# Performance work log

Measured on AMD Instinct MI355X. Metric: run time of the kernel, lower is better.

The kernel has to match this reference:

```python
import jax, jax.numpy as jnp
import numpy as np

# --- static config (matches init_kwargs) ---
N = 30000            # n_nodes
H = 8                # num_heads
OT = 16              # out_time_dim
OS = 240             # out_space_dim
IN_DIM = 16 + 1 + 240   # in_time+1 + in_space = 257
OUT_DIM = OT + 1 + OS   # 257 per head
BETA = -1.0
EPS = 1e-8
MAX_NORM = 1.0e6
SQRT_BETA = float(np.sqrt(abs(BETA)))


def setup_inputs() -> dict:
    key = jax.random.key(0)
    ks = jax.random.split(key, 7)
    def w(k, shape, fan_in):
        return (jax.random.normal(k, shape, jnp.float32) / np.sqrt(fan_in)).astype(jnp.float32)
    return {
        "query_input": jax.random.normal(ks[0], (N, IN_DIM), jnp.float32),
        "source_input": jax.random.normal(ks[1], (N, IN_DIM), jnp.float32),
        # stacked per-head PseudoLinear2 weights: [H, out, in]
        "Wq": w(ks[2], (H, OUT_DIM, IN_DIM), IN_DIM),
        "Wk": w(ks[3], (H, OUT_DIM, IN_DIM), IN_DIM),
        "Wv": w(ks[4], (H, OUT_DIM, IN_DIM), IN_DIM),
        # final head-concat projections (nn.Linear, bias=False): [out, in]
        "Ws": w(ks[5], (OT + 1, H * (OT + 1)), H * (OT + 1)),
        "Wh": w(ks[6], (OS, H * OS), H * OS),
    }


def _pseudo_linear(x, W):
    # Per-head linear; spherical block renormalized to radius sqrt(|beta|)
    # (hr output on the product manifold S^OT x H^OS). [N,D] x [H,O,D] -> [N,H,O]
    y = jnp.einsum('nd,hod->nho', x, W)
    s, sp = y[..., :OT + 1], y[..., OT + 1:]
    s = s * (SQRT_BETA / (jnp.linalg.norm(s, axis=-1, keepdims=True) + EPS))
    return jnp.concatenate([s, sp], axis=-1)


def _linear_attention(q, k, v, den_eps):
    # elu+1 feature-map linear attention; associative kv outer product per head.
    phi_q = jax.nn.elu(q) + 1.0
    phi_k = jax.nn.elu(k) + 1.0
    ktv = jnp.einsum('nhm,nhd->hmd', phi_k, v)          # [H,m,d]
    num = jnp.einsum('nhm,hmd->nhd', phi_q, ktv)        # [N,H,d]
    den = jnp.einsum('nhd,hd->nh', phi_q, phi_k.sum(0)) # [N,H]
    return num / (den[..., None] + den_eps)


def _l2norm(x):
    # torch F.normalize(p=2, dim=-1)
    return x / jnp.clip(jnp.linalg.norm(x, axis=-1, keepdims=True), 1e-12)


def reference(query_input, source_input, Wq, Wk, Wv, Ws, Wh):
    q = _pseudo_linear(query_input, Wq)   # [N,H,257]
    k = _pseudo_linear(source_input, Wk)
    v = _pseudo_linear(source_input, Wv)
    qs, qh = q[..., :OT + 1], q[..., OT + 1:]
    ks_, kh = k[..., :OT + 1], k[..., OT + 1:]
    vs, vh = v[..., :OT + 1], v[..., OT + 1:]

    # ---- spherical linear attention ----
    a = _linear_attention(qs, ks_, vs, 1e-6)            # [N,H,OT+1]
    a = a.reshape(N, H * (OT + 1)) @ Ws.T               # heads_concat
    an = jnp.linalg.norm(a, axis=-1, keepdims=True) + EPS
    mask = (an > MAX_NORM).astype(a.dtype)
    an_c = jnp.minimum(an, MAX_NORM)
    a_ = (a / an_c) * mask + a * (1.0 - mask)
    att_s = SQRT_BETA * _l2norm(a_)                     # [N,OT+1]

    # ---- hyperbolic linear attention ----
    b = _linear_attention(qh, kh, vh, 1e-8)             # [N,H,OS]
    b = b.reshape(N, H * OS) @ Wh.T
    bn = jnp.linalg.norm(b, axis=-1, keepdims=True) + EPS
    maskb = (bn > MAX_NORM).astype(b.dtype)
    bn_c = jnp.minimum(bn, MAX_NORM)
    b_ = _l2norm(b / bn_c) * MAX_NORM
    b2 = b_ * maskb + b * (1.0 - maskb)
    bt = jnp.sqrt(bn_c ** 2 - BETA)                     # hyperbolic time coord
    att_h = jnp.concatenate([bt, b2], axis=-1)          # [N,OS+1]

    out = jnp.concatenate([att_s, att_h], axis=-1)      # [N,OT+1+OS+1]
    # sh_to_q: product S x H -> pseudo-hyperboloid Q; reverse_extrinsic_map = identity here.
    s_part, h_part = out[:, :OT + 1], out[:, OT + 1:]
    q_out = jnp.concatenate([h_part[:, :1] * s_part / SQRT_BETA, h_part[:, 1:]], axis=-1)
    return q_out  # [N, 257]
```

## Files before the change

kernel.cpp:

```cpp
#include <hip/hip_runtime.h>
#include <math.h>

typedef __bf16 bf16_t;
typedef __bf16 bf16x8 __attribute__((ext_vector_type(8)));
typedef float f32x4 __attribute__((ext_vector_type(4)));

#define H    8
#define SD   17
#define HD   240
#define KIN  257
#define KQP  288
#define SCOL 256
#define DTOT 2176
#define NTOT 30000
#define CHS  15000
#define NCS  2
#define CHPS 15360
#define CHQ  15000
#define NCQ  2
#define YQROWS 15104
#define XROWS 15360
#define KSPLIT 16
#define OSPLIT 4
#define OSLAB (15104L * 257)

#define BK   32

__device__ __forceinline__ float phi_elu1(float x) {
    return x > 0.f ? x + 1.f : __expf(x);
}

__device__ __forceinline__ int xcd_swz(int orig, int nwg) {
    int q = nwg >> 3, r = nwg & 7;
    int xcd = orig & 7, off = orig >> 3;
    return (xcd < r ? xcd * (q + 1) : r * (q + 1) + (xcd - r) * q) + off;
}

__device__ __forceinline__ void gl_lds16(const bf16_t* g, bf16_t* l) {
    __builtin_amdgcn_global_load_lds(
        (const __attribute__((address_space(1))) void*)g,
        (__attribute__((address_space(3))) void*)l, 16, 0, 0);
}

template<int N> __device__ __forceinline__ void waitvm() {
    asm volatile("s_waitcnt vmcnt(%0)" :: "n"(N) : "memory");
    __builtin_amdgcn_sched_barrier(0);
}

struct GemmP {
    const bf16_t* A; long lda; long aHead;
    const bf16_t* B; long ldb; long bHead;
    float* Cf; bf16_t* Cb; long ldc; long cHead; int atomicC;
    int M, N, K, nSplit;
};

template<int TBM, int TBN>
__global__ void __launch_bounds__(256)
k_mfma_nt(GemmP p)
{
    constexpr int FI = TBM / 32;
    constexpr int FJ = TBN / 32;
    constexpr int LPT = TBM / 64 + TBN / 64;
    __shared__ bf16_t As[3][TBM * BK];
    __shared__ bf16_t Bs[3][TBN * BK];
    const int t  = threadIdx.x;
    const int z  = blockIdx.z;
    const int h  = z / p.nSplit;
    const int sp = z % p.nSplit;
    const int kWin = p.K / p.nSplit;
    const int k0   = sp * kWin;
    const int nwg  = gridDim.x * gridDim.y;
    const int wg   = xcd_swz(blockIdx.y * gridDim.x + blockIdx.x, nwg);
    const int m0 = (wg % gridDim.x) * TBM;
    const int n0 = (wg / gridDim.x) * TBN;
    const bf16_t* A = p.A + (long)h * p.aHead;
    const bf16_t* B = p.B + (long)h * p.bHead;

    const int lr = t >> 2;
    const int lc = t & 3;
    const int wid  = t >> 6;
    const int lane = t & 63;
    const int wm = (wid >> 1) * (TBM / 2);
    const int wn = (wid & 1) * (TBN / 2);
    const int fr = lane & 15;
    const int fq = lane >> 4;

    f32x4 acc[FI][FJ] = {};

    auto stage = [&](int buf, int kb) {
        const int gk = kb + ((lc ^ ((lr >> 1) & 3)) << 3);
#pragma unroll
        for (int it = 0; it < TBM / 64; ++it)
            gl_lds16(A + (long)(m0 + lr + it * 64) * p.lda + gk, &As[buf][it * 2048 + t * 8]);
#pragma unroll
        for (int it = 0; it < TBN / 64; ++it)
            gl_lds16(B + (long)(n0 + lr + it * 64) * p.ldb + gk, &Bs[buf][it * 2048 + t * 8]);
    };

    const int nSteps = kWin / BK;
    stage(0, k0);
    if (nSteps > 1) stage(1, k0 + BK);
    int cur = 0, pf = 2;
#pragma unroll 1
    for (int s = 0; s < nSteps; ++s) {
        if (s + 1 < nSteps) waitvm<LPT>();
        else                waitvm<0>();
        __builtin_amdgcn_s_barrier();
        __builtin_amdgcn_sched_barrier(0);
        if (s + 2 < nSteps) {
            stage(pf, k0 + (s + 2) * BK);
            pf = (pf == 2) ? 0 : pf + 1;
        }
        bf16x8 af[FI], bfr[FJ];
#pragma unroll
        for (int i = 0; i < FI; ++i) {
            const int row = wm + i * 16 + fr;
            af[i] = *(const bf16x8*)(&As[cur][row * BK + ((fq ^ ((row >> 1) & 3)) << 3)]);
        }
#pragma unroll
        for (int j = 0; j < FJ; ++j) {
            const int row = wn + j * 16 + fr;
            bfr[j] = *(const bf16x8*)(&Bs[cur][row * BK + ((fq ^ ((row >> 1) & 3)) << 3)]);
        }
#pragma unroll
        for (int i = 0; i < FI; ++i)
#pragma unroll
            for (int j = 0; j < FJ; ++j)
                acc[i][j] = __builtin_amdgcn_mfma_f32_16x16x32_bf16(af[i], bfr[j], acc[i][j], 0, 0, 0);
        cur = (cur == 2) ? 0 : cur + 1;
    }

    float*  Cf = 0; bf16_t* Cb = 0;
    if (p.atomicC == 3)      Cf = p.Cf + (long)z * p.cHead;
    else if (p.Cf)           Cf = p.Cf + (long)h * p.cHead;
    else                     Cb = p.Cb + (long)h * p.cHead;
#pragma unroll
    for (int i = 0; i < FI; ++i) {
#pragma unroll
        for (int r = 0; r < 4; ++r) {
            const int m = m0 + wm + i * 16 + fq * 4 + r;
            if (m >= p.M) continue;
#pragma unroll
            for (int j = 0; j < FJ; ++j) {
                const int n = n0 + wn + j * 16 + fr;
                if (n >= p.N) continue;
                const float v = acc[i][j][r];
                const long idx = (long)m * p.ldc + n;
                if (p.atomicC == 1)      atomicAdd(&Cf[idx], v);
                else if (Cf)             Cf[idx] = v;
                else                     Cb[idx] = (bf16_t)v;
            }
        }
    }
}

__global__ void __launch_bounds__(256)
k_mfma_kv(const bf16_t* __restrict__ A, const bf16_t* __restrict__ Bsrc,
          bf16_t* __restrict__ Tk, bf16_t* __restrict__ Tv,
          float* __restrict__ ksum, int nRows)
{
    constexpr int FI = 4, FJ = 4;
    constexpr int LPT = 4;
    __shared__ bf16_t As[3][128 * BK];
    __shared__ bf16_t Bs[3][128 * BK];
    const int t = threadIdx.x;
    const int nwg = gridDim.x * gridDim.y;
    const int wg  = xcd_swz(blockIdx.y * gridDim.x + blockIdx.x, nwg);
    const int m0 = (wg % gridDim.x) * 128;
    const int n0 = (wg / gridDim.x) * 128;

    const int lr = t >> 2;
    const int lc = t & 3;
    const int wid  = t >> 6;
    const int lane = t & 63;
    const int wm = (wid >> 1) * 64;
    const int wn = (wid & 1) * 64;
    const int fr = lane & 15;
    const int fq = lane >> 4;

    f32x4 acc[FI][FJ] = {};

    auto stage = [&](int buf, int kb) {
        const int gk = kb + ((lc ^ ((lr >> 1) & 3)) << 3);
        gl_lds16(A    + (long)(m0 + lr)      * KQP + gk, &As[buf][t * 8]);
        gl_lds16(A    + (long)(m0 + lr + 64) * KQP + gk, &As[buf][2048 + t * 8]);
        gl_lds16(Bsrc + (long)(n0 + lr)      * KQP + gk, &Bs[buf][t * 8]);
        gl_lds16(Bsrc + (long)(n0 + lr + 64) * KQP + gk, &Bs[buf][2048 + t * 8]);
    };

    constexpr int nSteps = KQP / BK;
    stage(0, 0);
    stage(1, BK);
    int cur = 0, pf = 2;
#pragma unroll 1
    for (int s = 0; s < nSteps; ++s) {
        if (s + 1 < nSteps) waitvm<LPT>();
        else                waitvm<0>();
        __builtin_amdgcn_s_barrier();
        __builtin_amdgcn_sched_barrier(0);
        if (s + 2 < nSteps) {
            stage(pf, (s + 2) * BK);
            pf = (pf == 2) ? 0 : pf + 1;
        }
        bf16x8 af[FI], bfr[FJ];
#pragma unroll
        for (int i = 0; i < FI; ++i) {
            const int row = wm + i * 16 + fr;
            af[i] = *(const bf16x8*)(&As[cur][row * BK + ((fq ^ ((row >> 1) & 3)) << 3)]);
        }
#pragma unroll
        for (int j = 0; j < FJ; ++j) {
            const int row = wn + j * 16 + fr;
            bfr[j] = *(const bf16x8*)(&Bs[cur][row * BK + ((fq ^ ((row >> 1) & 3)) << 3)]);
        }
#pragma unroll
        for (int i = 0; i < FI; ++i)
#pragma unroll
            for (int j = 0; j < FJ; ++j)
                acc[i][j] = __builtin_amdgcn_mfma_f32_16x16x32_bf16(af[i], bfr[j], acc[i][j], 0, 0, 0);
        cur = (cur == 2) ? 0 : cur + 1;
    }

    const bool isKh = (m0 >= SCOL) && (m0 < DTOT);
    bf16_t* outB = (m0 < DTOT) ? (Tk + (long)m0 * CHPS)
                               : (Tv + (long)(m0 - DTOT) * CHPS);
#pragma unroll
    for (int i = 0; i < FI; ++i) {
#pragma unroll
        for (int r = 0; r < 4; ++r) {
            const int ml = wm + i * 16 + fq * 4 + r;
            bf16_t* row = outB + (long)ml * CHPS;
            float kacc = 0.f;
#pragma unroll
            for (int j = 0; j < FJ; ++j) {
                const int n = n0 + wn + j * 16 + fr;
                float v = 0.f;
                if (n < nRows) {
                    v = acc[i][j][r];
                    if (isKh) { v = phi_elu1(v); kacc += v; }
                }
                row[n] = (bf16_t)v;
            }
            if (isKh) {
                kacc += __shfl_xor(kacc, 1);
                kacc += __shfl_xor(kacc, 2);
                kacc += __shfl_xor(kacc, 4);
                kacc += __shfl_xor(kacc, 8);
                if (fr == 0) atomicAdd(&ksum[m0 + ml], kacc);
            }
        }
    }
}

__global__ void __launch_bounds__(256)
k_post_kv_t(bf16_t* __restrict__ Tk, bf16_t* __restrict__ Tv,
            float* __restrict__ ksum, int rows)
{
    const int h = blockIdx.y;
    const int n = blockIdx.x * 256 + threadIdx.x;
    const int lane = threadIdx.x & 63;
    const bool act = n < rows;
    float kv[SD], vv[SD];
    float sk = 0.f, sv = 0.f;
#pragma unroll
    for (int j = 0; j < SD; ++j) {
        kv[j] = act ? (float)Tk[(long)(h * 32 + j) * CHPS + n] : 0.f;
        vv[j] = act ? (float)Tv[(long)(h * 32 + j) * CHPS + n] : 0.f;
        sk += kv[j] * kv[j];
        sv += vv[j] * vv[j];
    }
    const float ik = 1.f / (sqrtf(sk) + 1e-8f);
    const float iv = 1.f / (sqrtf(sv) + 1e-8f);
#pragma unroll
    for (int j = 0; j < SD; ++j) {
        float pk = act ? phi_elu1(kv[j] * ik) : 0.f;
        if (act) {
            Tk[(long)(h * 32 + j) * CHPS + n] = (bf16_t)pk;
            Tv[(long)(h * 32 + j) * CHPS + n] = (bf16_t)(vv[j] * iv);
        }
        float s = pk;
#pragma unroll
        for (int off = 32; off > 0; off >>= 1) s += __shfl_down(s, off);
        if (lane == 0) atomicAdd(&ksum[h * 32 + j], s);
    }
}

__global__ void k_cast_pad(const float* __restrict__ in, bf16_t* __restrict__ out, long rows)
{
    long i = (long)blockIdx.x * 256 + threadIdx.x;
    if (i >= rows * (KQP / 8)) return;
    long r = i / (KQP / 8); int c8 = (int)(i - r * (KQP / 8)) * 8;
    const float* ip = in + r * KIN + c8;
    bf16x8 o;
#pragma unroll
    for (int j = 0; j < 8; ++j)
        o[j] = (c8 + j < KIN) ? (bf16_t)ip[j] : (bf16_t)0.f;
    *(bf16x8*)(out + r * KQP + c8) = o;
}

__global__ void k_prep_proj(const float* __restrict__ W, bf16_t* __restrict__ dst)
{
    long i = (long)blockIdx.x * 256 + threadIdx.x;
    if (i >= (long)DTOT * KQP) return;
    int r = (int)(i / KQP), k = (int)(i % KQP);
    float v = 0.f;
    if (r < SCOL) {
        int h = r >> 5, j = r & 31;
        if (j < SD && k < KIN) v = W[((long)h * 257 + j) * 257 + k];
    } else {
        int rr = r - SCOL;
        int h = rr / HD, j = rr % HD;
        if (k < KIN) v = W[((long)h * 257 + SD + j) * 257 + k];
    }
    dst[i] = (bf16_t)v;
}

__global__ void k_prep_ws(const float* __restrict__ ws, bf16_t* __restrict__ out)
{
    int o = blockIdx.x; int t = threadIdx.x;
    int h = t >> 5, j = t & 31;
    float v = 0.f;
    if (o < SD && j < SD) v = ws[o * (H * SD) + h * SD + j];
    out[o * 256 + t] = (bf16_t)v;
}

__global__ void k_prep_wh(const float* __restrict__ wh, bf16_t* __restrict__ out)
{
    long i = (long)blockIdx.x * 256 + threadIdx.x;
    if (i >= 256L * 2048) return;
    int o = (int)(i / 2048), c = (int)(i % 2048);
    int h = c >> 8, j = c & 255;
    float v = 0.f;
    if (o < 240 && j < HD) v = wh[(long)o * 1920 + h * HD + j];
    out[i] = (bf16_t)v;
}

__global__ void __launch_bounds__(256)
k_post_q(bf16_t* __restrict__ Yq, const float* __restrict__ ksum, int rows)
{
    const int wid  = blockIdx.x * 4 + (threadIdx.x >> 6);
    const int lane = threadIdx.x & 63;
    const int n = wid >> 3, h = wid & 7;
    if (n >= rows) return;
    bf16_t* row = Yq + (long)n * DTOT;
    float qv = (lane < SD) ? (float)row[h * 32 + lane] : 0.f;
    float sq = qv * qv;
#pragma unroll
    for (int off = 32; off > 0; off >>= 1) sq += __shfl_down(sq, off);
    sq = __shfl(sq, 0);
    const float iq = 1.f / (sqrtf(sq) + 1e-8f);
    float pvs = (lane < SD) ? phi_elu1(qv * iq) : 0.f;
    float ds = (lane < SD) ? pvs * ksum[h * 32 + lane] : 0.f;
    float ph[8];
    float dh = 0.f;
    if (lane < 30) {
        bf16x8 hv8 = *(const bf16x8*)(row + SCOL + h * HD + lane * 8);
        const float* kp = ksum + SCOL + h * HD + lane * 8;
#pragma unroll
        for (int i = 0; i < 8; ++i) {
            ph[i] = phi_elu1((float)hv8[i]);
            dh += ph[i] * kp[i];
        }
    }
#pragma unroll
    for (int off = 32; off > 0; off >>= 1) {
        ds += __shfl_down(ds, off);
        dh += __shfl_down(dh, off);
    }
    ds = __shfl(ds, 0); dh = __shfl(dh, 0);
    const float ss = 1.f / (ds + 1e-6f);
    const float sh = 1.f / (dh + 1e-8f);
    if (lane < 32)
        row[h * 32 + lane] = (bf16_t)((lane < SD) ? pvs * ss : 0.f);
    if (lane < 30) {
        bf16x8 o8;
#pragma unroll
        for (int i = 0; i < 8; ++i) o8[i] = (bf16_t)(ph[i] * sh);
        *(bf16x8*)(row + SCOL + h * HD + lane * 8) = o8;
    }
}

__global__ void k_castf(const float* __restrict__ in, bf16_t* __restrict__ out, long n)
{
    long i = (long)blockIdx.x * 256 + threadIdx.x;
    if (i < n) out[i] = (bf16_t)in[i];
}

__global__ void __launch_bounds__(256)
k_finalize(const float* __restrict__ pre, float* __restrict__ outp, int rows)
{
    int n    = blockIdx.x * 4 + (threadIdx.x >> 6);
    int lane = threadIdx.x & 63;
    if (n >= rows) return;
    const float* rp = pre + (long)n * 257;
    float* op = outp + (long)n * 257;
    float sv = 0.f;
    if (lane < SD) {
#pragma unroll
        for (int s = 0; s < OSPLIT; ++s) sv += rp[s * OSLAB + lane];
    }
    float ssq = sv * sv;
    float hv[4];
    float hsq = 0.f;
#pragma unroll
    for (int i = 0; i < 4; ++i) {
        int o = lane + 64 * i;
        float v = 0.f;
        if (o < HD) {
#pragma unroll
            for (int s = 0; s < OSPLIT; ++s) v += rp[s * OSLAB + SD + o];
        }
        hv[i] = v;
        hsq += v * v;
    }
#pragma unroll
    for (int off = 32; off > 0; off >>= 1) {
        ssq += __shfl_down(ssq, off);
        hsq += __shfl_down(hsq, off);
    }
    ssq = __shfl(ssq, 0); hsq = __shfl(hsq, 0);
    float an_raw = sqrtf(ssq);
    float bn_raw = sqrtf(hsq);
    float an = an_raw + 1e-8f;
    float bn = bn_raw + 1e-8f;
    bool ma = an > 1e6f;
    bool mb = bn > 1e6f;
    float an_c = fminf(an, 1e6f);
    float bn_c = fminf(bn, 1e6f);
    float na = ma ? (an_raw / an_c) : an_raw;
    na = fmaxf(na, 1e-12f);
    float inv_s = (ma ? (1.f / an_c) : 1.f) / na;
    float bt = sqrtf(bn_c * bn_c + 1.0f);
    float nb = fmaxf(bn_raw / bn_c, 1e-12f);
    float scale_b = 1e6f / (bn_c * nb);
    if (lane < SD) op[lane] = bt * (sv * inv_s);
#pragma unroll
    for (int i = 0; i < 4; ++i) {
        int o = lane + 64 * i;
        if (o < HD) op[SD + o] = mb ? hv[i] * scale_b : hv[i];
    }
}

static inline long alup(long b) { return (b + 255) & ~255L; }

extern "C" void kernel_launch(void* const* d_in, const int* in_sizes, int n_in,
                              void* d_out, int out_size, void* d_ws, size_t ws_size,
                              hipStream_t stream)
{
    const float* query  = (const float*)d_in[0];
    const float* source = (const float*)d_in[1];
    const float* Wq     = (const float*)d_in[2];
    const float* Wk     = (const float*)d_in[3];
    const float* Wv     = (const float*)d_in[4];
    const float* Ws     = (const float*)d_in[5];
    const float* Wh     = (const float*)d_in[6];
    float* out = (float*)d_out;

    char* p = (char*)d_ws;
    auto alloc = [&](long b) { char* r = p; p += alup(b); return r; };
    bf16_t* Wkvb = (bf16_t*)alloc(2L * DTOT * KQP * 2);
    bf16_t* Wqb  = (bf16_t*)alloc((long)DTOT * KQP * 2);
    bf16_t* Wsb  = (bf16_t*)alloc(64L * 256 * 2);
    bf16_t* Whb  = (bf16_t*)alloc(256L * 2048 * 2);
    bf16_t* Gfull= (bf16_t*)alloc(384L * DTOT * 2);
    float*  ktvF = (float*) alloc((8L * HD * 256 + 8L * 32 * 32) * 4);
    float*  ksum = (float*) alloc((long)DTOT * 4);
    bf16_t* ktvB = (bf16_t*)alloc((8L * HD * 256 + 8L * 32 * 32) * 2);
    bf16_t* xcb  = (bf16_t*)alloc((long)XROWS * KQP * 2);
    long tkBytes = (long)DTOT * CHPS * 2;
    char* ub = alloc(2 * tkBytes + 16L * CHPS * 2);
    bf16_t* Tk  = (bf16_t*)ub;
    bf16_t* Tv  = Tk + (long)DTOT * CHPS;
    bf16_t* Yq  = Tk;
    float*  opre= (float*)(Yq + (long)YQROWS * DTOT);

    float*  ktvHf = ktvF;
    float*  ktvSf = ktvF + 8L * HD * 256;
    bf16_t* ktvHb = ktvB;
    bf16_t* ktvSb = ktvB + 8L * HD * 256;

    (void)hipMemsetAsync(ktvF, 0, (char*)(ksum + DTOT) - (char*)ktvF, stream);
    (void)hipMemsetAsync(Gfull, 0, 384L * DTOT * 2, stream);

    const unsigned gw = (unsigned)(((long)DTOT * KQP + 255) / 256);
    k_prep_proj<<<gw, 256, 0, stream>>>(Wk, Wkvb);
    k_prep_proj<<<gw, 256, 0, stream>>>(Wv, Wkvb + (long)DTOT * KQP);
    k_prep_proj<<<gw, 256, 0, stream>>>(Wq, Wqb);
    k_prep_ws<<<64, 256, 0, stream>>>(Ws, Wsb);
    k_prep_wh<<<(unsigned)((256L * 2048 + 255) / 256), 256, 0, stream>>>(Wh, Whb);

    GemmP g;

    for (int c = 0; c < NCS; ++c) {
        const float* src = source + (long)c * CHS * KIN;
        k_cast_pad<<<(unsigned)(((long)CHS * (KQP / 8) + 255) / 256), 256, 0, stream>>>(src, xcb, CHS);
        k_mfma_kv<<<dim3((2 * DTOT) / 128, CHPS / 128, 1), 256, 0, stream>>>(
            Wkvb, xcb, Tk, Tv, ksum, CHS);
        k_post_kv_t<<<dim3((CHS + 255) / 256, H), 256, 0, stream>>>(Tk, Tv, ksum, CHS);
        g = { Tk + (long)SCOL * CHPS, CHPS, (long)HD * CHPS,
              Tv + (long)SCOL * CHPS, CHPS, (long)HD * CHPS,
              ktvHf, 0, 256, (long)HD * 256, 1,  HD, HD, CHPS, KSPLIT };
        k_mfma_nt<128, 128><<<dim3(2, 2, H * KSPLIT), 256, 0, stream>>>(g);
        g = { Tk, CHPS, 32L * CHPS,  Tv, CHPS, 32L * CHPS,
              ktvSf, 0, 32, 32L * 32, 1,  32, 32, CHPS, KSPLIT };
        k_mfma_nt<64, 64><<<dim3(1, 1, H * KSPLIT), 256, 0, stream>>>(g);
    }
    k_castf<<<(unsigned)((8L * (HD * 256 + 32 * 32) + 255) / 256), 256, 0, stream>>>(
        ktvF, ktvB, 8L * (HD * 256 + 32 * 32));

    g = { Wsb, 256, 32,  ktvSb, 32, 32L * 32,  0, Gfull, DTOT, 32, 0,
          SD, 32, 32, 1 };
    k_mfma_nt<64, 64><<<dim3(1, 1, H), 256, 0, stream>>>(g);
    g = { Whb, 2048, 256,  ktvHb, 256, (long)HD * 256,
          0, Gfull + 17L * DTOT + SCOL, DTOT, HD, 0,
          HD, HD, 256, 1 };
    k_mfma_nt<64, 64><<<dim3(4, 4, H), 256, 0, stream>>>(g);

    for (int c = 0; c < NCQ; ++c) {
        const float* qsrc = query + (long)c * CHQ * KIN;
        float* orow = out + (long)c * CHQ * 257;
        k_cast_pad<<<(unsigned)(((long)CHQ * (KQP / 8) + 255) / 256), 256, 0, stream>>>(qsrc, xcb, CHQ);
        g = { xcb, KQP, 0,  Wqb, KQP, 0,  0, Yq, DTOT, 0, 0,
              CHQ, DTOT, KQP, 1 };
        k_mfma_nt<128, 128><<<dim3((CHQ + 127) / 128, DTOT / 128, 1), 256, 0, stream>>>(g);
        k_post_q<<<(CHQ * H) / 4, 256, 0, stream>>>(Yq, ksum, CHQ);
        g = { Yq, DTOT, 0,  Gfull, DTOT, 0,  opre, 0, 257, OSLAB, 3,
              CHQ, 257, DTOT, OSPLIT };
        k_mfma_nt<64, 192><<<dim3((CHQ + 63) / 64, 2, OSPLIT), 256, 0, stream>>>(g);
        k_finalize<<<(CHQ + 3) / 4, 256, 0, stream>>>(opre, orow, CHQ);
    }
}
```

Baseline: 948.6 us.

## Load MFMA fragments directly from global memory, bypassing LDS, in projection GEMMs

Adds an LDS-free variant of the NT GEMM where each wave loads its bf16x8 MFMA fragments straight from global memory into registers, double-buffered in registers, with no barriers. The K/V projection kernel and the Q projection GEMM switch to this path. It removes LDS staging, barriers and the shared-memory footprint, which may raise occupancy. In exchange, tiles are reloaded redundantly across waves, and global loads become strided 16-byte accesses that rely on L1/L2 for reuse.

```diff
diff --git a/kernel.cpp b/kernel.cpp
--- a/kernel.cpp
+++ b/kernel.cpp
@@ -54,15 +54,13 @@
     int M, N, K, nSplit;
 };
 
-template<int TBM, int TBN>
+template<int TBM, int TBN, int NBUF = 3>
 __global__ void __launch_bounds__(256)
 k_mfma_nt(GemmP p)
 {
     constexpr int FI = TBM / 32;
     constexpr int FJ = TBN / 32;
     constexpr int LPT = TBM / 64 + TBN / 64;
-    __shared__ bf16_t As[3][TBM * BK];
-    __shared__ bf16_t Bs[3][TBN * BK];
     const int t  = threadIdx.x;
     const int z  = blockIdx.z;
     const int h  = z / p.nSplit;
@@ -86,48 +84,81 @@
     const int fq = lane >> 4;
 
     f32x4 acc[FI][FJ] = {};
-
-    auto stage = [&](int buf, int kb) {
-        const int gk = kb + ((lc ^ ((lr >> 1) & 3)) << 3);
-#pragma unroll
-        for (int it = 0; it < TBM / 64; ++it)
-            gl_lds16(A + (long)(m0 + lr + it * 64) * p.lda + gk, &As[buf][it * 2048 + t * 8]);
-#pragma unroll
-        for (int it = 0; it < TBN / 64; ++it)
-            gl_lds16(B + (long)(n0 + lr + it * 64) * p.ldb + gk, &Bs[buf][it * 2048 + t * 8]);
-    };
-
     const int nSteps = kWin / BK;
-    stage(0, k0);
-    if (nSteps > 1) stage(1, k0 + BK);
-    int cur = 0, pf = 2;
+
+    if constexpr (NBUF == 0) {
+        const bf16_t* aB = A + (long)(m0 + wm + fr) * p.lda + fq * 8 + k0;
+        const bf16_t* bB = B + (long)(n0 + wn + fr) * p.ldb + fq * 8 + k0;
+        bf16x8 a0[FI], b0[FJ], a1[FI], b1[FJ];
+        auto ld = [&](bf16x8* as, bf16x8* bs, int kb) {
+#pragma unroll
+            for (int i = 0; i < FI; ++i)
+                as[i] = *(const bf16x8*)(aB + (long)i * 16 * p.lda + kb);
+#pragma unroll
+            for (int j = 0; j < FJ; ++j)
+                bs[j] = *(const bf16x8*)(bB + (long)j * 16 * p.ldb + kb);
+        };
+        auto mm = [&](bf16x8* as, bf16x8* bs) {
+#pragma unroll
+            for (int i = 0; i < FI; ++i)
+#pragma unroll
+                for (int j = 0; j < FJ; ++j)
+                    acc[i][j] = __builtin_amdgcn_mfma_f32_16x16x32_bf16(as[i], bs[j], acc[i][j], 0, 0, 0);
+        };
+        ld(a0, b0, 0);
 #pragma unroll 1
-    for (int s = 0; s < nSteps; ++s) {
-        if (s + 1 < nSteps) waitvm<LPT>();
-        else                waitvm<0>();
-        __builtin_amdgcn_s_barrier();
-        __builtin_amdgcn_sched_barrier(0);
-        if (s + 2 < nSteps) {
-            stage(pf, k0 + (s + 2) * BK);
-            pf = (pf == 2) ? 0 : pf + 1;
-        }
-        bf16x8 af[FI], bfr[FJ];
-#pragma unroll
-        for (int i = 0; i < FI; ++i) {
-            const int row = wm + i * 16 + fr;
-            af[i] = *(const bf16x8*)(&As[cur][row * BK + ((fq ^ ((row >> 1) & 3)) << 3)]);
-        }
-#pragma unroll
-        for (int j = 0; j < FJ; ++j) {
-            const int row = wn + j * 16 + fr;
-            bfr[j] = *(const bf16x8*)(&Bs[cur][row * BK + ((fq ^ ((row >> 1) & 3)) << 3)]);
-        }
-#pragma unroll
-        for (int i = 0; i < FI; ++i)
-#pragma unroll
-            for (int j = 0; j < FJ; ++j)
-                acc[i][j] = __builtin_amdgcn_mfma_f32_16x16x32_bf16(af[i], bfr[j], acc[i][j], 0, 0, 0);
-        cur = (cur == 2) ? 0 : cur + 1;
+        for (int s = 0; s < nSteps; s += 2) {
+            if (s + 1 < nSteps) ld(a1, b1, (s + 1) * BK);
+            mm(a0, b0);
+            if (s + 2 < nSteps) ld(a0, b0, (s + 2) * BK);
+            if (s + 1 < nSteps) mm(a1, b1);
+        }
+    } else {
+        __shared__ bf16_t As[NBUF ? NBUF : 1][TBM * BK];
+        __shared__ bf16_t Bs[NBUF ? NBUF : 1][TBN * BK];
+        auto stage = [&](int buf, int kb) {
+            const int gk = kb + ((lc ^ ((lr >> 1) & 3)) << 3);
+#pragma unroll
+            for (int it = 0; it < TBM / 64; ++it)
+                gl_lds16(A + (long)(m0 + lr + it * 64) * p.lda + gk, &As[buf][it * 2048 + t * 8]);
+#pragma unroll
+            for (int it = 0; it < TBN / 64; ++it)
+                gl_lds16(B + (long)(n0 + lr + it * 64) * p.ldb + gk, &Bs[buf][it * 2048 + t * 8]);
+        };
+        auto compute = [&](int cur) {
+            bf16x8 af[FI], bfr[FJ];
+#pragma unroll
+            for (int i = 0; i < FI; ++i) {
+                const int row = wm + i * 16 + fr;
+                af[i] = *(const bf16x8*)(&As[cur][row * BK + ((fq ^ ((row >> 1) & 3)) << 3)]);
+            }
+#pragma unroll
+            for (int j = 0; j < FJ; ++j) {
+                const int row = wn + j * 16 + fr;
+                bfr[j] = *(const bf16x8*)(&Bs[cur][row * BK + ((fq ^ ((row >> 1) & 3)) << 3)]);
+            }
+#pragma unroll
+            for (int i = 0; i < FI; ++i)
+#pragma unroll
+                for (int j = 0; j < FJ; ++j)
+                    acc[i][j] = __builtin_amdgcn_mfma_f32_16x16x32_bf16(af[i], bfr[j], acc[i][j], 0, 0, 0);
+        };
+        stage(0, k0);
+        if (nSteps > 1) stage(1, k0 + BK);
+        int cur = 0, pf = 2;
+#pragma unroll 1
+        for (int s = 0; s < nSteps; ++s) {
+            if (s + 1 < nSteps) waitvm<LPT>();
+            else                waitvm<0>();
+            __builtin_amdgcn_s_barrier();
+            __builtin_amdgcn_sched_barrier(0);
+            if (s + 2 < nSteps) {
+                stage(pf, k0 + (s + 2) * BK);
+                pf = (pf == 2) ? 0 : pf + 1;
+            }
+            compute(cur);
+            cur = (cur == 2) ? 0 : cur + 1;
+        }
     }
 
     float*  Cf = 0; bf16_t* Cb = 0;
@@ -160,17 +191,12 @@
           float* __restrict__ ksum, int nRows)
 {
     constexpr int FI = 4, FJ = 4;
-    constexpr int LPT = 4;
-    __shared__ bf16_t As[3][128 * BK];
-    __shared__ bf16_t Bs[3][128 * BK];
     const int t = threadIdx.x;
     const int nwg = gridDim.x * gridDim.y;
     const int wg  = xcd_swz(blockIdx.y * gridDim.x + blockIdx.x, nwg);
     const int m0 = (wg % gridDim.x) * 128;
     const int n0 = (wg / gridDim.x) * 128;
 
-    const int lr = t >> 2;
-    const int lc = t & 3;
     const int wid  = t >> 6;
     const int lane = t & 63;
     const int wm = (wid >> 1) * 64;
@@ -179,46 +205,33 @@
     const int fq = lane >> 4;
 
     f32x4 acc[FI][FJ] = {};
-
-    auto stage = [&](int buf, int kb) {
-        const int gk = kb + ((lc ^ ((lr >> 1) & 3)) << 3);
-        gl_lds16(A    + (long)(m0 + lr)      * KQP + gk, &As[buf][t * 8]);
-        gl_lds16(A    + (long)(m0 + lr + 64) * KQP + gk, &As[buf][2048 + t * 8]);
-        gl_lds16(Bsrc + (long)(n0 + lr)      * KQP + gk, &Bs[buf][t * 8]);
-        gl_lds16(Bsrc + (long)(n0 + lr + 64) * KQP + gk, &Bs[buf][2048 + t * 8]);
+    const bf16_t* aB = A    + (long)(m0 + wm + fr) * KQP + fq * 8;
+    const bf16_t* bB = Bsrc + (long)(n0 + wn + fr) * KQP + fq * 8;
+
+    bf16x8 a0[FI], b0[FJ], a1[FI], b1[FJ];
+    auto ld = [&](bf16x8* as, bf16x8* bs, int kb) {
+#pragma unroll
+        for (int i = 0; i < FI; ++i)
+            as[i] = *(const bf16x8*)(aB + (long)i * 16 * KQP + kb);
+#pragma unroll
+        for (int j = 0; j < FJ; ++j)
+            bs[j] = *(const bf16x8*)(bB + (long)j * 16 * KQP + kb);
     };
-
+    auto mm = [&](bf16x8* as, bf16x8* bs) {
+#pragma unroll
+        for (int i = 0; i < FI; ++i)
+#pragma unroll
+            for (int j = 0; j < FJ; ++j)
+                acc[i][j] = __builtin_amdgcn_mfma_f32_16x16x32_bf16(as[i], bs[j], acc[i][j], 0, 0, 0);
+    };
     constexpr int nSteps = KQP / BK;
-    stage(0, 0);
-    stage(1, BK);
-    int cur = 0, pf = 2;
+    ld(a0, b0, 0);
 #pragma unroll 1
-    for (int s = 0; s < nSteps; ++s) {
-        if (s + 1 < nSteps) waitvm<LPT>();
-        else                waitvm<0>();
-        __builtin_amdgcn_s_barrier();
-        __builtin_amdgcn_sched_barrier(0);
-        if (s + 2 < nSteps) {
-            stage(pf, (s + 2) * BK);
-            pf = (pf == 2) ? 0 : pf + 1;
-        }
-        bf16x8 af[FI], bfr[FJ];
-#pragma unroll
-        for (int i = 0; i < FI; ++i) {
-            const int row = wm + i * 16 + fr;
-            af[i] = *(const bf16x8*)(&As[cur][row * BK + ((fq ^ ((row >> 1) & 3)) << 3)]);
-        }
-#pragma unroll
-        for (int j = 0; j < FJ; ++j) {
-            const int row = wn + j * 16 + fr;
-            bfr[j] = *(const bf16x8*)(&Bs[cur][row * BK + ((fq ^ ((row >> 1) & 3)) << 3)]);
-        }
-#pragma unroll
-        for (int i = 0; i < FI; ++i)
-#pragma unroll
-            for (int j = 0; j < FJ; ++j)
-                acc[i][j] = __builtin_amdgcn_mfma_f32_16x16x32_bf16(af[i], bfr[j], acc[i][j], 0, 0, 0);
-        cur = (cur == 2) ? 0 : cur + 1;
+    for (int s = 0; s < nSteps; s += 2) {
+        if (s + 1 < nSteps) ld(a1, b1, (s + 1) * BK);
+        mm(a0, b0);
+        if (s + 2 < nSteps) ld(a0, b0, (s + 2) * BK);
+        if (s + 1 < nSteps) mm(a1, b1);
     }
 
     const bool isKh = (m0 >= SCOL) && (m0 < DTOT);
@@ -522,7 +535,7 @@
         k_cast_pad<<<(unsigned)(((long)CHQ * (KQP / 8) + 255) / 256), 256, 0, stream>>>(qsrc, xcb, CHQ);
         g = { xcb, KQP, 0,  Wqb, KQP, 0,  0, Yq, DTOT, 0, 0,
               CHQ, DTOT, KQP, 1 };
-        k_mfma_nt<128, 128><<<dim3((CHQ + 127) / 128, DTOT / 128, 1), 256, 0, stream>>>(g);
+        k_mfma_nt<128, 128, 0><<<dim3((CHQ + 127) / 128, DTOT / 128, 1), 256, 0, stream>>>(g);
         k_post_q<<<(CHQ * H) / 4, 256, 0, stream>>>(Yq, ksum, CHQ);
         g = { Yq, DTOT, 0,  Gfull, DTOT, 0,  opre, 0, 257, OSLAB, 3,
               CHQ, 257, DTOT, OSPLIT };
```

Measured after the change: 1.029 ms. 8.4% more time.
